# Performance work log

Measured on AMD Instinct MI355X. Metric: run time of the kernel, lower is better.

Reference implementation:

```python
import jax, jax.numpy as jnp
import numpy as np

B, F, SF = 2, 5, 15          # batch, query frames, num_shots*sframe
C, KD, VD = 1024, 128, 512   # encoder_dim, keydim, valdim
H = W = 32                   # l3 feature map (output stride 8 on 256x256)


def _conv(x, w, b, pad):
    y = jax.lax.conv_general_dilated(
        x, w, window_strides=(1, 1), padding=[(pad, pad), (pad, pad)],
        dimension_numbers=("NCHW", "OIHW", "NCHW"))
    return y + b[None, :, None, None]


def setup_inputs() -> dict:
    key = jax.random.key(0)
    ks = jax.random.split(key, 8)
    s = 0.02
    return {
        "query_feat": jax.random.normal(ks[0], (B * F, C, H, W), jnp.float32),
        "support_fg_feat": jax.random.normal(ks[1], (B * SF, C, H, W), jnp.float32),
        "w_sk": jax.random.normal(ks[2], (KD, C, 3, 3), jnp.float32) * s,
        "b_sk": jnp.zeros((KD,), jnp.float32),
        "w_sv": jax.random.normal(ks[3], (VD, C, 3, 3), jnp.float32) * s,
        "b_sv": jnp.zeros((VD,), jnp.float32),
        "w_qq": jax.random.normal(ks[4], (KD, C, 3, 3), jnp.float32) * s,
        "b_qq": jnp.zeros((KD,), jnp.float32),
        "w_qk": jax.random.normal(ks[5], (KD, C, 3, 3), jnp.float32) * s,
        "b_qk": jnp.zeros((KD,), jnp.float32),
        "w_cq": jax.random.normal(ks[6], (VD, C, 1, 1), jnp.float32) * s,
        "b_cq": jnp.zeros((VD,), jnp.float32),
    }


def reference(query_feat, support_fg_feat, w_sk, b_sk, w_sv, b_sv,
              w_qq, b_qq, w_qk, b_qk, w_cq, b_cq):
    hw = H * W
    # QKV projections (3x3 convs)
    sk = _conv(support_fg_feat, w_sk, b_sk, 1)   # [B*SF, KD, H, W]
    sv = _conv(support_fg_feat, w_sv, b_sv, 1)   # [B*SF, VD, H, W]
    qq = _conv(query_feat, w_qq, b_qq, 1)        # [B*F, KD, H, W]
    qk = _conv(query_feat, w_qk, b_qk, 1)        # [B*F, KD, H, W]

    # support K: [B, SF*hw, KD];  support V: [B, VD, SF*hw]
    support_k = sk.reshape(B, SF, KD, H, W).transpose(0, 2, 1, 3, 4)
    support_k = support_k.reshape(B, KD, SF * hw).transpose(0, 2, 1)
    support_v = sv.reshape(B, SF, VD, H, W).transpose(0, 2, 1, 3, 4)
    support_v = support_v.reshape(B, VD, SF * hw)

    qq5 = qq.reshape(B, F, KD, H, W)
    qk5 = qk.reshape(B, F, KD, H, W)
    mid = F // 2
    scale = 1.0 / jnp.sqrt(jnp.float32(KD))

    # stage 1: middle-frame query attends into support memory
    middle_q = qq5[:, mid].reshape(B, KD, hw)                 # [B, KD, hw]
    P1 = jnp.einsum("bkc,bcq->bkq", support_k, middle_q) * scale  # [B, SF*hw, hw]
    P1 = jax.nn.softmax(P1, axis=1)
    new_V = jnp.einsum("bvk,bkq->bvq", support_v, P1)          # [B, VD, hw]

    # stage 2: all-frame queries attend into middle-frame keys
    middle_K = qk5[:, mid].reshape(B, KD, hw).transpose(0, 2, 1)   # [B, hw, KD]
    qq_flat = qq5.transpose(0, 2, 1, 3, 4).reshape(B, KD, F * hw)  # [B, KD, F*hw]
    P2 = jnp.einsum("bkc,bcq->bkq", middle_K, qq_flat) * scale     # [B, hw, F*hw]
    P2 = jax.nn.softmax(P2, axis=1)
    Out = jnp.einsum("bvk,bkq->bvq", new_V, P2)                    # [B, VD, F*hw]

    after = Out.reshape(B, VD, F, H, W).transpose(0, 2, 1, 3, 4)
    after = after.reshape(B * F, VD, H, W)
    qf = _conv(query_feat, w_cq, b_cq, 0)                          # [B*F, VD, H, W]
    return jnp.concatenate([after, qf], axis=1)                    # [B*F, 2*VD, H, W]
```

## Files before the change

kernel.cpp:

```cpp
#include <hip/hip_runtime.h>
#include <cstdint>

typedef unsigned short u16;
typedef __attribute__((ext_vector_type(8))) u16 u16x8;
typedef __attribute__((ext_vector_type(4))) u16 u16x4;
typedef __attribute__((ext_vector_type(8))) _Float16 f16x8;
typedef __attribute__((ext_vector_type(4))) float f32x4;

__device__ __forceinline__ u16 f2h(float f) {
  _Float16 h = (_Float16)f;
  return __builtin_bit_cast(u16, h);
}
__device__ __forceinline__ float h2f(u16 b) {
  _Float16 h = __builtin_bit_cast(_Float16, b);
  return (float)h;
}
__device__ __forceinline__ void gll16(const void* g, void* l) {
  auto gp = reinterpret_cast<const __attribute__((address_space(1))) unsigned int*>(
      reinterpret_cast<uintptr_t>(g));
  auto lp = reinterpret_cast<__attribute__((address_space(3))) unsigned int*>(
      reinterpret_cast<uintptr_t>(l));
  __builtin_amdgcn_global_load_lds(gp, lp, 16, 0, 0);
}

__global__ __launch_bounds__(256) void pad_both(const float* __restrict__ qsrc,
                                                const float* __restrict__ ssrc,
                                                u16* __restrict__ PQ,
                                                u16* __restrict__ PS) {
  const int gi = blockIdx.x >> 5;
  const int y  = blockIdx.x & 31;
  const float* in;
  u16* outp;
  int img;
  if (gi < 10) { in = qsrc; outp = PQ; img = gi; }
  else         { in = ssrc; outp = PS; img = gi - 10; }
  __shared__ float tile[32][33];
  const int tid = threadIdx.x;
  u16* base = outp + (long)img * 34 * 34 * 1024;
  const u16x8 z8 = {0, 0, 0, 0, 0, 0, 0, 0};
  {
    u16* r = base + (long)(y + 1) * 34 * 1024;
    if (tid < 128) *(u16x8*)&r[tid * 8] = z8;
    else *(u16x8*)&r[33 * 1024 + (tid - 128) * 8] = z8;
  }
  if (y == 0) {
    for (int i = tid * 8; i < 34816; i += 2048) *(u16x8*)&base[i] = z8;
  }
  if (y == 31) {
    u16* r = base + 33L * 34 * 1024;
    for (int i = tid * 8; i < 34816; i += 2048) *(u16x8*)&r[i] = z8;
  }
  const int xi = tid & 31, ci = tid >> 5;
  const int xo = tid >> 3, q = tid & 7;
  const float* ip = in + (long)img * 1048576 + y * 32;
  u16* op = base + ((long)(y + 1) * 34 + 1) * 1024;
  for (int c0 = 0; c0 < 1024; c0 += 32) {
#pragma unroll
    for (int k2 = 0; k2 < 4; k2++)
      tile[k2 * 8 + ci][xi] = ip[(long)(c0 + k2 * 8 + ci) * 1024 + xi];
    __syncthreads();
    u16x4 o4;
#pragma unroll
    for (int r = 0; r < 4; r++) o4[r] = f2h(tile[q * 4 + r][xo]);
    *(u16x4*)&op[(long)xo * 1024 + c0 + q * 4] = o4;
    __syncthreads();
  }
}

__device__ __forceinline__ void wre3_body(const float* __restrict__ wp,
                                          u16* __restrict__ op, float* buf) {
  for (int i = threadIdx.x; i < 9216; i += 256) buf[i] = wp[i];
  __syncthreads();
  for (int k = threadIdx.x; k < 9216; k += 256) {
    const int cblk = k / 576;
    const int r = k - cblk * 576;
    const int t = r >> 6, ci = r & 63;
    op[k] = f2h(buf[(cblk * 64 + ci) * 9 + t]);
  }
}
__global__ __launch_bounds__(256) void wprep(
    const float* __restrict__ w_sk, const float* __restrict__ w_sv,
    const float* __restrict__ w_qq, const float* __restrict__ w_qk,
    const float* __restrict__ w_cq, u16* __restrict__ WTSK,
    u16* __restrict__ WTSV, u16* __restrict__ WTQQK, u16* __restrict__ WCQ) {
  __shared__ float buf[9216];
  const int b = blockIdx.x;
  if (b < 128) {
    wre3_body(w_sk + (long)b * 9216, WTSK + (long)b * 9216, buf);
  } else if (b < 640) {
    const int oc = b - 128;
    wre3_body(w_sv + (long)oc * 9216, WTSV + (long)oc * 9216, buf);
  } else if (b < 768) {
    const int oc = b - 640;
    wre3_body(w_qq + (long)oc * 9216, WTQQK + (long)oc * 9216, buf);
  } else if (b < 896) {
    const int oc = b - 768;
    wre3_body(w_qk + (long)oc * 9216, WTQQK + (long)(oc + 128) * 9216, buf);
  } else {
    const int i = (b - 896) * 1024 + threadIdx.x * 4;
#pragma unroll
    for (int r = 0; r < 4; r++) WCQ[i + r] = f2h(w_cq[i + r]);
  }
}

__global__ __launch_bounds__(64) void reduceD(const float* __restrict__ ps,
                                              float* __restrict__ D, int NT) {
  const int row = blockIdx.x, tid = threadIdx.x;
  const float* p = ps + (long)row * NT;
  float s = (tid < NT) ? p[tid] : 0.f;
  if (tid + 64 < NT) s += p[tid + 64];
#pragma unroll
  for (int o = 32; o > 0; o >>= 1) s += __shfl_xor(s, o, 64);
  if (tid == 0) D[row] = s;
}

__global__ __launch_bounds__(256) void reduce8h(const u16* __restrict__ part,
                                                const float* __restrict__ D,
                                                u16* __restrict__ o) {
  long j = ((long)blockIdx.x * 256 + threadIdx.x) * 4;
  int b = (int)(j >> 19);
  long i = j & 524287;
  int q = (int)(i & 1023);
  const u16* p = part + (long)b * 4194304 + i;
  float s0 = 0.f, s1 = 0.f, s2 = 0.f, s3 = 0.f;
#pragma unroll
  for (int c = 0; c < 8; c++) {
    u16x4 v = *(const u16x4*)&p[(long)c * 524288];
    s0 += h2f(v[0]); s1 += h2f(v[1]); s2 += h2f(v[2]); s3 += h2f(v[3]);
  }
  f32x4 dv = *(const f32x4*)&D[b * 1024 + q];
  u16x4 o4 = {f2h(s0 / dv[0]), f2h(s1 / dv[1]), f2h(s2 / dv[2]),
              f2h(s3 / dv[3])};
  *(u16x4*)&o[j] = o4;
}
__global__ __launch_bounds__(256) void reduce_sk(const u16* __restrict__ part,
                                                 const float* __restrict__ bias,
                                                 u16* __restrict__ o) {
  long i = ((long)blockIdx.x * 256 + threadIdx.x) * 4;
  u16x4 a = *(const u16x4*)&part[i];
  u16x4 b = *(const u16x4*)&part[i + 3932160];
  f32x4 bb = *(const f32x4*)&bias[(int)(i & 127)];
  u16x4 o4;
#pragma unroll
  for (int r = 0; r < 4; r++) o4[r] = f2h(h2f(a[r]) + h2f(b[r]) + bb[r]);
  *(u16x4*)&o[i] = o4;
}
__global__ __launch_bounds__(256) void reduce_qqk(
    const u16* __restrict__ part, const float* __restrict__ b_qq,
    const float* __restrict__ b_qk, u16* __restrict__ QQR,
    u16* __restrict__ QKR) {
  long i = ((long)blockIdx.x * 256 + threadIdx.x) * 4;
  const int n = (int)(i >> 8), m = (int)(i & 255);
  u16x4 a = *(const u16x4*)&part[i];
  u16x4 b = *(const u16x4*)&part[i + 2621440];
  const int lo = (m < 128);
  const int mm = m & 127;
  const float* bs = lo ? b_qq : b_qk;
  f32x4 bb = *(const f32x4*)&bs[mm];
  u16* dst = (lo ? QQR : QKR) + (long)n * 128 + mm;
  u16x4 o4;
#pragma unroll
  for (int r = 0; r < 4; r++) o4[r] = f2h(h2f(a[r]) + h2f(b[r]) + bb[r]);
  *(u16x4*)dst = o4;
}

__global__ __launch_bounds__(512, 1)
void gemm256(const u16* __restrict__ A, const u16* __restrict__ B,
             const float* __restrict__ bias, u16* __restrict__ out) {
  __shared__ u16 lds[81920];
  const int tid = threadIdx.x, lane = tid & 63, wave = tid >> 6;
  const int nwg = gridDim.x * gridDim.y;
  int wg = blockIdx.x + gridDim.x * blockIdx.y;
  wg = (wg & 7) * (nwg >> 3) + (wg >> 3);
  const int ntile = wg % gridDim.x;
  const int mtile = wg / gridDim.x;

  const int slog = (lane & 7) ^ ((lane >> 3) & 7);
  const u16* aS[4];
  const u16* bS[4];
  int aD[4], bD[4];
#pragma unroll
  for (int j = 0; j < 4; j++) {
    const int r = wave * 32 + j * 8 + (lane >> 3);
    aS[j] = A + (long)(mtile * 256 + r) * 9216 + slog * 8;
    aD[j] = (wave * 32 + j * 8) * 64;
    const int n = ntile * 256 + r;
    const int img = n >> 10, p = n & 1023;
    const int y = p >> 5, x = p & 31;
    bS[j] = B + ((long)((img * 34 + y) * 34 + x)) * 1024 + slog * 8;
    bD[j] = (wave * 32 + j * 8) * 64;
  }

  const int g = lane >> 4, l15 = lane & 15;
  const int wm = wave >> 2, wn = wave & 3;
  int aRow[8], bRow[4], sx[2];
#pragma unroll
  for (int mi = 0; mi < 8; mi++) aRow[mi] = (wm * 128 + mi * 16 + l15) * 64;
#pragma unroll
  for (int ni = 0; ni < 4; ni++) bRow[ni] = (wn * 64 + ni * 16 + l15) * 64;
#pragma unroll
  for (int ks = 0; ks < 2; ks++) sx[ks] = ((ks * 4 + g) ^ (l15 & 7)) * 8;

  auto conv_badd = [](int kt) {
    const int cblk = kt / 9;
    const int t = kt - cblk * 9;
    const int dy = t / 3, dx = t - dy * 3;
    return (dy * 34 + dx) * 1024 + cblk * 64;
  };

  f32x4 acc[8][4];
  const f32x4 zero = {0.f, 0.f, 0.f, 0.f};
#pragma unroll
  for (int i = 0; i < 8; i++)
#pragma unroll
    for (int j = 0; j < 4; j++) acc[i][j] = zero;

  const int nkt = 144;
  {
#pragma unroll
    for (int j = 0; j < 4; j++) gll16(aS[j], &lds[aD[j]]);
    const int b0o = conv_badd(0), b1o = conv_badd(1);
#pragma unroll
    for (int j = 0; j < 4; j++) gll16(bS[j] + b0o, &lds[32768 + bD[j]]);
#pragma unroll
    for (int j = 0; j < 4; j++) gll16(bS[j] + b1o, &lds[49152 + bD[j]]);
    asm volatile("s_waitcnt vmcnt(4)" ::: "memory");
    __builtin_amdgcn_s_barrier();
  }

  f16x8 a0[4], a1[4], a3[4], b0[4], b2[4];
  f16x8 zf;
#pragma unroll
  for (int j = 0; j < 8; j++) zf[j] = (_Float16)0.0f;
#pragma unroll
  for (int i = 0; i < 4; i++) { a3[i] = zf; b2[i] = zf; }

  int bc = 0;
  for (int kt = 0; kt < nkt; ++kt) {
    const int abuf = (kt & 1) << 14;
    const int anbuf = abuf ^ 16384;
    const int bbuf = 32768 + bc * 16384;
    int bsn = bc + 2; if (bsn >= 3) bsn -= 3;
    const int bnbuf = 32768 + bsn * 16384;
    const bool stA = (kt + 1 < nkt);
    const bool stB = (kt + 2 < nkt);
    const int kA = (kt + 1) << 6;
    const int bAdd2 = stB ? conv_badd(kt + 2) : 0;

#pragma unroll
    for (int i = 0; i < 4; i++) a0[i] = *(const f16x8*)&lds[abuf + aRow[i] + sx[0]];
#pragma unroll
    for (int i = 0; i < 4; i++) b0[i] = *(const f16x8*)&lds[bbuf + bRow[i] + sx[0]];
#pragma unroll
    for (int i = 0; i < 4; i++) a1[i] = *(const f16x8*)&lds[abuf + aRow[i + 4] + sx[0]];
#pragma unroll
    for (int mi = 0; mi < 4; mi++)
#pragma unroll
      for (int ni = 0; ni < 4; ni++)
        acc[mi + 4][ni] = __builtin_amdgcn_mfma_f32_16x16x32_f16(
            a3[mi], b2[ni], acc[mi + 4][ni], 0, 0, 0);
    if (stA) {
#pragma unroll
      for (int j = 0; j < 4; j++) gll16(aS[j] + kA, &lds[anbuf + aD[j]]);
    }
#pragma unroll
    for (int mi = 0; mi < 4; mi++)
#pragma unroll
      for (int ni = 0; ni < 4; ni++)
        acc[mi][ni] = __builtin_amdgcn_mfma_f32_16x16x32_f16(
            a0[mi], b0[ni], acc[mi][ni], 0, 0, 0);
#pragma unroll
    for (int i = 0; i < 4; i++) a0[i] = *(const f16x8*)&lds[abuf + aRow[i] + sx[1]];
#pragma unroll
    for (int i = 0; i < 4; i++) b2[i] = *(const f16x8*)&lds[bbuf + bRow[i] + sx[1]];
    if (stB) {
#pragma unroll
      for (int j = 0; j < 4; j++) gll16(bS[j] + bAdd2, &lds[bnbuf + bD[j]]);
    }
#pragma unroll
    for (int mi = 0; mi < 4; mi++)
#pragma unroll
      for (int ni = 0; ni < 4; ni++)
        acc[mi + 4][ni] = __builtin_amdgcn_mfma_f32_16x16x32_f16(
            a1[mi], b0[ni], acc[mi + 4][ni], 0, 0, 0);
#pragma unroll
    for (int i = 0; i < 4; i++) a3[i] = *(const f16x8*)&lds[abuf + aRow[i + 4] + sx[1]];
#pragma unroll
    for (int mi = 0; mi < 4; mi++)
#pragma unroll
      for (int ni = 0; ni < 4; ni++)
        acc[mi][ni] = __builtin_amdgcn_mfma_f32_16x16x32_f16(
            a0[mi], b2[ni], acc[mi][ni], 0, 0, 0);
    if (stB) {
      asm volatile("s_waitcnt vmcnt(4)" ::: "memory");
    } else if (stA) {
      asm volatile("s_waitcnt vmcnt(0)" ::: "memory");
    }
    __builtin_amdgcn_s_barrier();
    bc = bc + 1; if (bc >= 3) bc -= 3;
  }
#pragma unroll
  for (int mi = 0; mi < 4; mi++)
#pragma unroll
    for (int ni = 0; ni < 4; ni++)
      acc[mi + 4][ni] = __builtin_amdgcn_mfma_f32_16x16x32_f16(
          a3[mi], b2[ni], acc[mi + 4][ni], 0, 0, 0);

#pragma unroll
  for (int mi = 0; mi < 8; mi++) {
#pragma unroll
    for (int ni = 0; ni < 4; ni++) {
      f32x4 v = acc[mi][ni];
      const int m0 = mtile * 256 + wm * 128 + mi * 16 + g * 4;
      const int n = ntile * 256 + wn * 64 + ni * 16 + l15;
      const int b = (n >= 15360) ? 1 : 0;
      const int rem = n - b * 15360;
#pragma unroll
      for (int r = 0; r < 4; r++) {
        const int m = m0 + r;
        out[(long)b * 7864320 + (long)m * 15360 + rem] = f2h(v[r] + bias[m]);
      }
    }
  }
}

template <int BMODE, int EPI, int SPLITK>
__global__ __launch_bounds__(256, 2)
void gemm_nt(const u16* __restrict__ A, long Azoff, int Astride,
             const u16* __restrict__ B, long Bzoff, int Bstride,
             int K, float scale,
             const float* __restrict__ bias, const float* __restrict__ bias2,
             void* __restrict__ out0, void* __restrict__ out1,
             long out_zoff, int ldo, float cexp = 0.f) {
  __shared__ u16 lds[4 * 8192];
  const int tid = threadIdx.x;
  const int lane = tid & 63;
  const int wave = tid >> 6;
  const int mtile = blockIdx.y, ntile = blockIdx.x, z = blockIdx.z;

  const int zb = (SPLITK > 1) ? z / SPLITK : z;
  const int zc = (SPLITK > 1) ? z % SPLITK : 0;
  const u16* Ab = A + (long)zb * Azoff + (long)zc * K;
  const u16* Bb = B + (long)zb * Bzoff + ((BMODE == 0) ? (long)zc * K : 0);

  const int r8 = lane >> 3;
  const int sphys = lane & 7;
  const u16* aSrc[4];
  const u16* bSrc[4];
  u16* aDst[4];
  u16* bDst[4];
#pragma unroll
  for (int i = 0; i < 4; i++) {
    const int row = wave * 32 + i * 8 + r8;
    const int slog = sphys ^ (row & 7);
    aSrc[i] = Ab + (long)(mtile * 128 + row) * Astride + slog * 8;
    if (BMODE == 0) {
      bSrc[i] = Bb + (long)(ntile * 128 + row) * Bstride + slog * 8;
    } else {
      const int n = ntile * 128 + row;
      const int img = n >> 10;
      const int p = n & 1023;
      const int y = p >> 5, x = p & 31;
      bSrc[i] = Bb + ((long)(img * 34 + y) * 34 + x) * 1024 + slog * 8;
    }
    aDst[i] = &lds[0] + (wave * 32 + i * 8) * 64;
    bDst[i] = &lds[0] + 8192 + (wave * 32 + i * 8) * 64;
  }

  const int g = lane >> 4, l15 = lane & 15;
  const int wm = wave >> 1, wn = wave & 1;
  int offA[2][4], offB[2][4];
#pragma unroll
  for (int ks = 0; ks < 2; ks++) {
    const int sl = ks * 4 + g;
#pragma unroll
    for (int i = 0; i < 4; i++) {
      const int ra = wm * 64 + i * 16 + l15;
      offA[ks][i] = ra * 64 + ((sl ^ (ra & 7)) * 8);
      const int rb = wn * 64 + i * 16 + l15;
      offB[ks][i] = 8192 + rb * 64 + ((sl ^ (rb & 7)) * 8);
    }
  }

  auto stage = [&](int buf, int kb) {
    int bAdd;
    if (BMODE == 0) {
      bAdd = kb;
    } else if (BMODE == 1) {
      const int ktg = (zc * K + kb) >> 6;
      const int cblk = ktg / 9;
      const int t = ktg - cblk * 9;
      const int dy = t / 3, dx = t - dy * 3;
      bAdd = (dy * 34 + dx) * 1024 + cblk * 64;
    } else {
      bAdd = 35 * 1024 + kb;
    }
    const int bufo = buf * 16384;
#pragma unroll
    for (int i = 0; i < 4; i++) gll16(aSrc[i] + kb, aDst[i] + bufo);
#pragma unroll
    for (int i = 0; i < 4; i++) gll16(bSrc[i] + bAdd, bDst[i] + bufo);
  };

  f32x4 acc[4][4];
  const f32x4 zero = {0.f, 0.f, 0.f, 0.f};
#pragma unroll
  for (int i = 0; i < 4; i++)
#pragma unroll
    for (int j = 0; j < 4; j++) acc[i][j] = zero;

  const int nkt = K >> 6;
  stage(0, 0);
  __syncthreads();
  for (int kt = 0; kt < nkt; ++kt) {
    const int buf = kt & 1;
    if (kt + 1 < nkt) stage(buf ^ 1, (kt + 1) << 6);
#pragma unroll
    for (int ks = 0; ks < 2; ks++) {
      f16x8 af[4], bfg[4];
#pragma unroll
      for (int i = 0; i < 4; i++)
        af[i] = *(const f16x8*)&lds[buf * 16384 + offA[ks][i]];
#pragma unroll
      for (int i = 0; i < 4; i++)
        bfg[i] = *(const f16x8*)&lds[buf * 16384 + offB[ks][i]];
#pragma unroll
      for (int mi = 0; mi < 4; mi++)
#pragma unroll
        for (int ni = 0; ni < 4; ni++)
          acc[mi][ni] = __builtin_amdgcn_mfma_f32_16x16x32_f16(
              af[mi], bfg[ni], acc[mi][ni], 0, 0, 0);
    }
    __syncthreads();
  }

  float rp[4][4];
  if (EPI == 7) {
#pragma unroll
    for (int a = 0; a < 4; a++)
#pragma unroll
      for (int b = 0; b < 4; b++) rp[a][b] = 0.f;
  }

#pragma unroll
  for (int mi = 0; mi < 4; mi++) {
#pragma unroll
    for (int ni = 0; ni < 4; ni++) {
      f32x4 v = acc[mi][ni];
      const int m0 = mtile * 128 + wm * 64 + mi * 16 + g * 4;
      const int n = ntile * 128 + wn * 64 + ni * 16 + l15;
      if (EPI == 0) {
        u16* ob = (u16*)out0;
        const float* bs = bias;
        int mm = m0;
        if (out1 != nullptr && m0 >= 128) { ob = (u16*)out1; bs = bias2; mm = m0 - 128; }
        u16x4 pk;
#pragma unroll
        for (int r = 0; r < 4; r++) {
          float val = v[r] * scale + (bs ? bs[mm + r] : 0.f);
          pk[r] = f2h(val);
        }
        *(u16x4*)&ob[(long)n * ldo + mm] = pk;
      } else if (EPI == 1) {
        u16* ob = (u16*)out0 + (long)z * out_zoff;
#pragma unroll
        for (int r = 0; r < 4; r++) {
          const int m = m0 + r;
          float val = v[r] * scale + (bias ? bias[m] : 0.f);
          ob[(long)m * ldo + n] = f2h(val);
        }
      } else if (EPI == 2) {
        float* of = (float*)out0;
        const int img = n >> 10, p = n & 1023;
#pragma unroll
        for (int r = 0; r < 4; r++) {
          const int m = m0 + r;
          of[(long)img * 1048576 + (long)(512 + m) * 1024 + p] =
              v[r] + (bias ? bias[m] : 0.f);
        }
      } else if (EPI == 3) {
        float* of = (float*)out0;
        const int f = n >> 10, p = n & 1023;
        const float dinv = 1.0f / bias2[(long)z * 5120 + n];
#pragma unroll
        for (int r = 0; r < 4; r++) {
          const int m = m0 + r;
          of[(long)z * 5242880 + (long)f * 1048576 + (long)m * 1024 + p] =
              v[r] * dinv;
        }
      } else if (EPI == 4) {
        float* of = (float*)out0 + (long)z * out_zoff;
#pragma unroll
        for (int r = 0; r < 4; r++) of[(long)(m0 + r) * ldo + n] = v[r];
      } else if (EPI == 5) {
        float* of = (float*)out0 + (long)zc * out_zoff;
        *(f32x4*)&of[(long)n * ldo + m0] = v;
      } else if (EPI == 6) {
        u16* ob = (u16*)out0 + (long)z * out_zoff;
#pragma unroll
        for (int r = 0; r < 4; r++) ob[(long)(m0 + r) * ldo + n] = f2h(v[r]);
      } else if (EPI == 7) {
        u16* ob = (u16*)out0 + (long)z * out_zoff;
#pragma unroll
        for (int r = 0; r < 4; r++) {
          const int m = m0 + r;
          float e = __expf(v[r] * scale - cexp);
          ob[(long)m * ldo + n] = f2h(e);
          rp[mi][r] += e;
        }
      } else {
        u16* ob = (u16*)out0 + (long)zc * out_zoff;
        u16x4 pk;
#pragma unroll
        for (int r = 0; r < 4; r++) pk[r] = f2h(v[r]);
        *(u16x4*)&ob[(long)n * ldo + m0] = pk;
      }
    }
  }

  if (EPI == 7) {
    float* ps = (float*)lds;
#pragma unroll
    for (int mi = 0; mi < 4; mi++) {
#pragma unroll
      for (int r = 0; r < 4; r++) {
        float s = rp[mi][r];
        s += __shfl_xor(s, 1, 64);
        s += __shfl_xor(s, 2, 64);
        s += __shfl_xor(s, 4, 64);
        s += __shfl_xor(s, 8, 64);
        if (l15 == 0) ps[wn * 128 + wm * 64 + mi * 16 + g * 4 + r] = s;
      }
    }
    __syncthreads();
    if (tid < 128) {
      float s = ps[tid] + ps[128 + tid];
      const int MR = gridDim.y << 7;
      float* PS = (float*)out1;
      PS[((long)z * MR + mtile * 128 + tid) * gridDim.x + ntile] = s;
    }
  }
}

extern "C" void kernel_launch(void* const* d_in, const int* in_sizes, int n_in,
                              void* d_out, int out_size, void* d_ws, size_t ws_size,
                              hipStream_t stream) {
  (void)in_sizes; (void)n_in; (void)out_size;
  const float* query   = (const float*)d_in[0];
  const float* support = (const float*)d_in[1];
  const float* w_sk = (const float*)d_in[2];  const float* b_sk = (const float*)d_in[3];
  const float* w_sv = (const float*)d_in[4];  const float* b_sv = (const float*)d_in[5];
  const float* w_qq = (const float*)d_in[6];  const float* b_qq = (const float*)d_in[7];
  const float* w_qk = (const float*)d_in[8];  const float* b_qk = (const float*)d_in[9];
  const float* w_cq = (const float*)d_in[10]; const float* b_cq = (const float*)d_in[11];
  float* out = (float*)d_out;
  char* ws = (char*)d_ws;

  if (ws_size < 158924800u) return;

  u16* PQ    = (u16*)(ws + 0);
  u16* PS    = (u16*)(ws + 23674880);
  u16* WTSK  = (u16*)(ws + 94699520);
  u16* WTSV  = (u16*)(ws + 97058816);
  u16* WTQQK = (u16*)(ws + 106496000);
  u16* WCQ   = (u16*)(ws + 111214592);
  u16* SKR   = (u16*)(ws + 112263168);
  u16* SVA   = (u16*)(ws + 120127488);
  u16* QQR   = (u16*)(ws + 151584768);
  u16* QKR   = (u16*)(ws + 154206208);
  u16* NEWV  = (u16*)(ws + 156827648);
  u16* P1T   = PS;
  u16* P2T   = PQ;
  u16* PART2 = (u16*)(ws + 94699520);
  u16* PARTKH = SVA;
  u16* PARTQH = SVA;
  float* PSUM1 = (float*)(ws + 97058816);
  float* PSUM2 = (float*)(ws + 94699520);
  float* D1 = (float*)(ws + 112263168);
  float* D2 = D1 + 2048;

  const float SCALE = 0.08838834764831843f;

  pad_both<<<dim3(1280), 256, 0, stream>>>(query, support, PQ, PS);
  wprep<<<dim3(1408), 256, 0, stream>>>(w_sk, w_sv, w_qq, w_qk, w_cq,
                                        WTSK, WTSV, WTQQK, WCQ);

  gemm_nt<1, 8, 2><<<dim3(240, 1, 2), 256, 0, stream>>>(
      WTSK, 0, 9216, PS, 0, 0, 4608, 1.0f, nullptr, nullptr, PARTKH, nullptr,
      3932160L, 128);
  reduce_sk<<<dim3(3840), 256, 0, stream>>>(PARTKH, b_sk, SKR);

  gemm_nt<1, 8, 2><<<dim3(80, 2, 2), 256, 0, stream>>>(
      WTQQK, 0, 9216, PQ, 0, 0, 4608, 1.0f, nullptr, nullptr, PARTQH, nullptr,
      2621440L, 256);
  reduce_qqk<<<dim3(2560), 256, 0, stream>>>(PARTQH, b_qq, b_qk, QQR, QKR);

  gemm256<<<dim3(120, 2), 512, 0, stream>>>(WTSV, PS, b_sv, SVA);

  gemm_nt<2, 2, 1><<<dim3(80, 4, 1), 256, 0, stream>>>(
      WCQ, 0, 1024, PQ, 0, 0, 1024, 1.0f, b_cq, nullptr, out, nullptr, 0, 0);

  gemm_nt<0, 7, 1><<<dim3(120, 8, 2), 256, 0, stream>>>(
      QQR + 262144, 655360L, 128, SKR, 1966080L, 128, 128, SCALE, nullptr,
      nullptr, P1T, PSUM1, 15728640L, 15360, 12.0f);
  reduceD<<<dim3(2048), 64, 0, stream>>>(PSUM1, D1, 120);
  gemm_nt<0, 6, 8><<<dim3(8, 4, 16), 256, 0, stream>>>(
      SVA, 7864320L, 15360, P1T, 15728640L, 15360, 1920, 1.0f, nullptr,
      nullptr, PART2, nullptr, 524288L, 1024);
  reduce8h<<<dim3(1024), 256, 0, stream>>>(PART2, D1, NEWV);

  gemm_nt<0, 7, 1><<<dim3(8, 40, 2), 256, 0, stream>>>(
      QQR, 655360L, 128, QKR + 262144, 655360L, 128, 128, SCALE, nullptr,
      nullptr, P2T, PSUM2, 5242880L, 1024, 10.0f);
  reduceD<<<dim3(10240), 64, 0, stream>>>(PSUM2, D2, 8);
  gemm_nt<0, 3, 1><<<dim3(40, 4, 2), 256, 0, stream>>>(
      NEWV, 524288L, 1024, P2T, 5242880L, 1024, 1024, 1.0f, nullptr, D2,
      out, nullptr, 0, 0);
}
```

Before: 595.5 us.

## Merge independent kernel launches into combined dual-role kernels

```diff
diff --git a/kernel.cpp b/kernel.cpp
--- a/kernel.cpp
+++ b/kernel.cpp
@@ -21,50 +21,6 @@
   auto lp = reinterpret_cast<__attribute__((address_space(3))) unsigned int*>(
       reinterpret_cast<uintptr_t>(l));
   __builtin_amdgcn_global_load_lds(gp, lp, 16, 0, 0);
-}
-
-__global__ __launch_bounds__(256) void pad_both(const float* __restrict__ qsrc,
-                                                const float* __restrict__ ssrc,
-                                                u16* __restrict__ PQ,
-                                                u16* __restrict__ PS) {
-  const int gi = blockIdx.x >> 5;
-  const int y  = blockIdx.x & 31;
-  const float* in;
-  u16* outp;
-  int img;
-  if (gi < 10) { in = qsrc; outp = PQ; img = gi; }
-  else         { in = ssrc; outp = PS; img = gi - 10; }
-  __shared__ float tile[32][33];
-  const int tid = threadIdx.x;
-  u16* base = outp + (long)img * 34 * 34 * 1024;
-  const u16x8 z8 = {0, 0, 0, 0, 0, 0, 0, 0};
-  {
-    u16* r = base + (long)(y + 1) * 34 * 1024;
-    if (tid < 128) *(u16x8*)&r[tid * 8] = z8;
-    else *(u16x8*)&r[33 * 1024 + (tid - 128) * 8] = z8;
-  }
-  if (y == 0) {
-    for (int i = tid * 8; i < 34816; i += 2048) *(u16x8*)&base[i] = z8;
-  }
-  if (y == 31) {
-    u16* r = base + 33L * 34 * 1024;
-    for (int i = tid * 8; i < 34816; i += 2048) *(u16x8*)&r[i] = z8;
-  }
-  const int xi = tid & 31, ci = tid >> 5;
-  const int xo = tid >> 3, q = tid & 7;
-  const float* ip = in + (long)img * 1048576 + y * 32;
-  u16* op = base + ((long)(y + 1) * 34 + 1) * 1024;
-  for (int c0 = 0; c0 < 1024; c0 += 32) {
-#pragma unroll
-    for (int k2 = 0; k2 < 4; k2++)
-      tile[k2 * 8 + ci][xi] = ip[(long)(c0 + k2 * 8 + ci) * 1024 + xi];
-    __syncthreads();
-    u16x4 o4;
-#pragma unroll
-    for (int r = 0; r < 4; r++) o4[r] = f2h(tile[q * 4 + r][xo]);
-    *(u16x4*)&op[(long)xo * 1024 + c0 + q * 4] = o4;
-    __syncthreads();
-  }
 }
 
 __device__ __forceinline__ void wre3_body(const float* __restrict__ wp,
@@ -78,40 +34,90 @@
     op[k] = f2h(buf[(cblk * 64 + ci) * 9 + t]);
   }
 }
-__global__ __launch_bounds__(256) void wprep(
+__global__ __launch_bounds__(256) void prep_all(
+    const float* __restrict__ qsrc, const float* __restrict__ ssrc,
+    u16* __restrict__ PQ, u16* __restrict__ PS,
     const float* __restrict__ w_sk, const float* __restrict__ w_sv,
     const float* __restrict__ w_qq, const float* __restrict__ w_qk,
     const float* __restrict__ w_cq, u16* __restrict__ WTSK,
     u16* __restrict__ WTSV, u16* __restrict__ WTQQK, u16* __restrict__ WCQ) {
   __shared__ float buf[9216];
-  const int b = blockIdx.x;
-  if (b < 128) {
-    wre3_body(w_sk + (long)b * 9216, WTSK + (long)b * 9216, buf);
-  } else if (b < 640) {
-    const int oc = b - 128;
-    wre3_body(w_sv + (long)oc * 9216, WTSV + (long)oc * 9216, buf);
-  } else if (b < 768) {
-    const int oc = b - 640;
-    wre3_body(w_qq + (long)oc * 9216, WTQQK + (long)oc * 9216, buf);
-  } else if (b < 896) {
-    const int oc = b - 768;
-    wre3_body(w_qk + (long)oc * 9216, WTQQK + (long)(oc + 128) * 9216, buf);
+  const int bb = blockIdx.x;
+  if (bb < 1280) {
+    const int gi = bb >> 5;
+    const int y  = bb & 31;
+    const float* in;
+    u16* outp;
+    int img;
+    if (gi < 10) { in = qsrc; outp = PQ; img = gi; }
+    else         { in = ssrc; outp = PS; img = gi - 10; }
+    float (*tile)[33] = (float(*)[33])buf;
+    const int tid = threadIdx.x;
+    u16* base = outp + (long)img * 34 * 34 * 1024;
+    const u16x8 z8 = {0, 0, 0, 0, 0, 0, 0, 0};
+    {
+      u16* r = base + (long)(y + 1) * 34 * 1024;
+      if (tid < 128) *(u16x8*)&r[tid * 8] = z8;
+      else *(u16x8*)&r[33 * 1024 + (tid - 128) * 8] = z8;
+    }
+    if (y == 0) {
+      for (int i = tid * 8; i < 34816; i += 2048) *(u16x8*)&base[i] = z8;
+    }
+    if (y == 31) {
+      u16* r = base + 33L * 34 * 1024;
+      for (int i = tid * 8; i < 34816; i += 2048) *(u16x8*)&r[i] = z8;
+    }
+    const int xi = tid & 31, ci = tid >> 5;
+    const int xo = tid >> 3, q = tid & 7;
+    const float* ip = in + (long)img * 1048576 + y * 32;
+    u16* op = base + ((long)(y + 1) * 34 + 1) * 1024;
+    for (int c0 = 0; c0 < 1024; c0 += 32) {
+#pragma unroll
+      for (int k2 = 0; k2 < 4; k2++)
+        tile[k2 * 8 + ci][xi] = ip[(long)(c0 + k2 * 8 + ci) * 1024 + xi];
+      __syncthreads();
+      u16x4 o4;
+#pragma unroll
+      for (int r = 0; r < 4; r++) o4[r] = f2h(tile[q * 4 + r][xo]);
+      *(u16x4*)&op[(long)xo * 1024 + c0 + q * 4] = o4;
+      __syncthreads();
+    }
   } else {
-    const int i = (b - 896) * 1024 + threadIdx.x * 4;
-#pragma unroll
-    for (int r = 0; r < 4; r++) WCQ[i + r] = f2h(w_cq[i + r]);
-  }
-}
-
-__global__ __launch_bounds__(64) void reduceD(const float* __restrict__ ps,
-                                              float* __restrict__ D, int NT) {
+    const int b = bb - 1280;
+    if (b < 128) {
+      wre3_body(w_sk + (long)b * 9216, WTSK + (long)b * 9216, buf);
+    } else if (b < 640) {
+      const int oc = b - 128;
+      wre3_body(w_sv + (long)oc * 9216, WTSV + (long)oc * 9216, buf);
+    } else if (b < 768) {
+      const int oc = b - 640;
+      wre3_body(w_qq + (long)oc * 9216, WTQQK + (long)oc * 9216, buf);
+    } else if (b < 896) {
+      const int oc = b - 768;
+      wre3_body(w_qk + (long)oc * 9216, WTQQK + (long)(oc + 128) * 9216, buf);
+    } else {
+      const int i = (b - 896) * 1024 + threadIdx.x * 4;
+#pragma unroll
+      for (int r = 0; r < 4; r++) WCQ[i + r] = f2h(w_cq[i + r]);
+    }
+  }
+}
+
+__global__ __launch_bounds__(64) void reduceDx(const float* __restrict__ ps1,
+                                               float* __restrict__ D1,
+                                               const float* __restrict__ ps2,
+                                               float* __restrict__ D2) {
   const int row = blockIdx.x, tid = threadIdx.x;
-  const float* p = ps + (long)row * NT;
+  const float* p;
+  float* D;
+  int NT;
+  if (row < 2048) { p = ps1 + (long)row * 120; D = D1 + row; NT = 120; }
+  else { const int r2 = row - 2048; p = ps2 + (long)r2 * 8; D = D2 + r2; NT = 8; }
   float s = (tid < NT) ? p[tid] : 0.f;
   if (tid + 64 < NT) s += p[tid + 64];
 #pragma unroll
   for (int o = 32; o > 0; o >>= 1) s += __shfl_xor(s, o, 64);
-  if (tid == 0) D[row] = s;
+  if (tid == 0) *D = s;
 }
 
 __global__ __launch_bounds__(256) void reduce8h(const u16* __restrict__ part,
@@ -133,35 +139,37 @@
               f2h(s3 / dv[3])};
   *(u16x4*)&o[j] = o4;
 }
-__global__ __launch_bounds__(256) void reduce_sk(const u16* __restrict__ part,
-                                                 const float* __restrict__ bias,
-                                                 u16* __restrict__ o) {
-  long i = ((long)blockIdx.x * 256 + threadIdx.x) * 4;
-  u16x4 a = *(const u16x4*)&part[i];
-  u16x4 b = *(const u16x4*)&part[i + 3932160];
-  f32x4 bb = *(const f32x4*)&bias[(int)(i & 127)];
-  u16x4 o4;
-#pragma unroll
-  for (int r = 0; r < 4; r++) o4[r] = f2h(h2f(a[r]) + h2f(b[r]) + bb[r]);
-  *(u16x4*)&o[i] = o4;
-}
-__global__ __launch_bounds__(256) void reduce_qqk(
-    const u16* __restrict__ part, const float* __restrict__ b_qq,
-    const float* __restrict__ b_qk, u16* __restrict__ QQR,
-    u16* __restrict__ QKR) {
-  long i = ((long)blockIdx.x * 256 + threadIdx.x) * 4;
-  const int n = (int)(i >> 8), m = (int)(i & 255);
-  u16x4 a = *(const u16x4*)&part[i];
-  u16x4 b = *(const u16x4*)&part[i + 2621440];
-  const int lo = (m < 128);
-  const int mm = m & 127;
-  const float* bs = lo ? b_qq : b_qk;
-  f32x4 bb = *(const f32x4*)&bs[mm];
-  u16* dst = (lo ? QQR : QKR) + (long)n * 128 + mm;
-  u16x4 o4;
-#pragma unroll
-  for (int r = 0; r < 4; r++) o4[r] = f2h(h2f(a[r]) + h2f(b[r]) + bb[r]);
-  *(u16x4*)dst = o4;
+__global__ __launch_bounds__(256) void reduce_kq(
+    const u16* __restrict__ partK, const float* __restrict__ b_sk,
+    u16* __restrict__ SKR, const u16* __restrict__ partQ,
+    const float* __restrict__ b_qq, const float* __restrict__ b_qk,
+    u16* __restrict__ QQR, u16* __restrict__ QKR) {
+  int blk = blockIdx.x;
+  if (blk < 3840) {
+    long i = ((long)blk * 256 + threadIdx.x) * 4;
+    u16x4 a = *(const u16x4*)&partK[i];
+    u16x4 b = *(const u16x4*)&partK[i + 3932160];
+    f32x4 bb = *(const f32x4*)&b_sk[(int)(i & 127)];
+    u16x4 o4;
+#pragma unroll
+    for (int r = 0; r < 4; r++) o4[r] = f2h(h2f(a[r]) + h2f(b[r]) + bb[r]);
+    *(u16x4*)&SKR[i] = o4;
+  } else {
+    blk -= 3840;
+    long i = ((long)blk * 256 + threadIdx.x) * 4;
+    const int n = (int)(i >> 8), m = (int)(i & 255);
+    u16x4 a = *(const u16x4*)&partQ[i];
+    u16x4 b = *(const u16x4*)&partQ[i + 2621440];
+    const int lo = (m < 128);
+    const int mm = m & 127;
+    const float* bs = lo ? b_qq : b_qk;
+    f32x4 bb = *(const f32x4*)&bs[mm];
+    u16* dst = (lo ? QQR : QKR) + (long)n * 128 + mm;
+    u16x4 o4;
+#pragma unroll
+    for (int r = 0; r < 4; r++) o4[r] = f2h(h2f(a[r]) + h2f(b[r]) + bb[r]);
+    *(u16x4*)dst = o4;
+  }
 }
 
 __global__ __launch_bounds__(512, 1)
@@ -325,18 +333,16 @@
 }
 
 template <int BMODE, int EPI, int SPLITK>
-__global__ __launch_bounds__(256, 2)
-void gemm_nt(const u16* __restrict__ A, long Azoff, int Astride,
-             const u16* __restrict__ B, long Bzoff, int Bstride,
-             int K, float scale,
-             const float* __restrict__ bias, const float* __restrict__ bias2,
-             void* __restrict__ out0, void* __restrict__ out1,
-             long out_zoff, int ldo, float cexp = 0.f) {
-  __shared__ u16 lds[4 * 8192];
+__device__ __forceinline__ void gemm_body(
+    int mtile, int ntile, int z, int NTd, int MRd,
+    const u16* __restrict__ A, long Azoff, int Astride,
+    const u16* __restrict__ B, long Bzoff, int Bstride,
+    int K, float scale, const float* __restrict__ bias,
+    const float* __restrict__ bias2, void* __restrict__ out0,
+    void* __restrict__ out1, long out_zoff, int ldo, float cexp, u16* lds) {
   const int tid = threadIdx.x;
   const int lane = tid & 63;
   const int wave = tid >> 6;
-  const int mtile = blockIdx.y, ntile = blockIdx.x, z = blockIdx.z;
 
   const int zb = (SPLITK > 1) ? z / SPLITK : z;
   const int zc = (SPLITK > 1) ? z % SPLITK : 0;
@@ -363,8 +369,8 @@
       const int y = p >> 5, x = p & 31;
       bSrc[i] = Bb + ((long)(img * 34 + y) * 34 + x) * 1024 + slog * 8;
     }
-    aDst[i] = &lds[0] + (wave * 32 + i * 8) * 64;
-    bDst[i] = &lds[0] + 8192 + (wave * 32 + i * 8) * 64;
+    aDst[i] = lds + (wave * 32 + i * 8) * 64;
+    bDst[i] = lds + 8192 + (wave * 32 + i * 8) * 64;
   }
 
   const int g = lane >> 4, l15 = lane & 15;
@@ -449,27 +455,7 @@
       f32x4 v = acc[mi][ni];
       const int m0 = mtile * 128 + wm * 64 + mi * 16 + g * 4;
       const int n = ntile * 128 + wn * 64 + ni * 16 + l15;
-      if (EPI == 0) {
-        u16* ob = (u16*)out0;
-        const float* bs = bias;
-        int mm = m0;
-        if (out1 != nullptr && m0 >= 128) { ob = (u16*)out1; bs = bias2; mm = m0 - 128; }
-        u16x4 pk;
-#pragma unroll
-        for (int r = 0; r < 4; r++) {
-          float val = v[r] * scale + (bs ? bs[mm + r] : 0.f);
-          pk[r] = f2h(val);
-        }
-        *(u16x4*)&ob[(long)n * ldo + mm] = pk;
-      } else if (EPI == 1) {
-        u16* ob = (u16*)out0 + (long)z * out_zoff;
-#pragma unroll
-        for (int r = 0; r < 4; r++) {
-          const int m = m0 + r;
-          float val = v[r] * scale + (bias ? bias[m] : 0.f);
-          ob[(long)m * ldo + n] = f2h(val);
-        }
-      } else if (EPI == 2) {
+      if (EPI == 2) {
         float* of = (float*)out0;
         const int img = n >> 10, p = n & 1023;
 #pragma unroll
@@ -488,13 +474,6 @@
           of[(long)z * 5242880 + (long)f * 1048576 + (long)m * 1024 + p] =
               v[r] * dinv;
         }
-      } else if (EPI == 4) {
-        float* of = (float*)out0 + (long)z * out_zoff;
-#pragma unroll
-        for (int r = 0; r < 4; r++) of[(long)(m0 + r) * ldo + n] = v[r];
-      } else if (EPI == 5) {
-        float* of = (float*)out0 + (long)zc * out_zoff;
-        *(f32x4*)&of[(long)n * ldo + m0] = v;
       } else if (EPI == 6) {
         u16* ob = (u16*)out0 + (long)z * out_zoff;
 #pragma unroll
@@ -535,10 +514,62 @@
     __syncthreads();
     if (tid < 128) {
       float s = ps[tid] + ps[128 + tid];
-      const int MR = gridDim.y << 7;
-      float* PS = (float*)out1;
-      PS[((long)z * MR + mtile * 128 + tid) * gridDim.x + ntile] = s;
-    }
+      float* PSp = (float*)out1;
+      PSp[((long)z * MRd + mtile * 128 + tid) * NTd + ntile] = s;
+    }
+  }
+}
+
+template <int BMODE, int EPI, int SPLITK>
+__global__ __launch_bounds__(256, 2)
+void gemm_nt(const u16* __restrict__ A, long Azoff, int Astride,
+             const u16* __restrict__ B, long Bzoff, int Bstride,
+             int K, float scale,
+             const float* __restrict__ bias, const float* __restrict__ bias2,
+             void* __restrict__ out0, void* __restrict__ out1,
+             long out_zoff, int ldo, float cexp = 0.f) {
+  __shared__ u16 lds[32768];
+  gemm_body<BMODE, EPI, SPLITK>(blockIdx.y, blockIdx.x, blockIdx.z,
+                                gridDim.x, gridDim.y << 7, A, Azoff, Astride,
+                                B, Bzoff, Bstride, K, scale, bias, bias2,
+                                out0, out1, out_zoff, ldo, cexp, lds);
+}
+
+__global__ __launch_bounds__(256, 2)
+void conv_dual(const u16* __restrict__ WTSK, const u16* __restrict__ WTQQK,
+               const u16* __restrict__ PS, const u16* __restrict__ PQ,
+               u16* __restrict__ PARTKH, u16* __restrict__ PARTQH) {
+  __shared__ u16 lds[32768];
+  int b = blockIdx.x;
+  if (b < 480) {
+    gemm_body<1, 8, 2>(0, b % 240, b / 240, 0, 0, WTSK, 0, 9216, PS, 0, 0,
+                       4608, 1.0f, nullptr, nullptr, PARTKH, nullptr,
+                       3932160L, 128, 0.f, lds);
+  } else {
+    b -= 480;
+    gemm_body<1, 8, 2>((b / 80) % 2, b % 80, b / 160, 0, 0, WTQQK, 0, 9216,
+                       PQ, 0, 0, 4608, 1.0f, nullptr, nullptr, PARTQH,
+                       nullptr, 2621440L, 256, 0.f, lds);
+  }
+}
+
+__global__ __launch_bounds__(256, 2)
+void pgemm_dual(const u16* __restrict__ QQR, const u16* __restrict__ SKR,
+                const u16* __restrict__ QKR, u16* __restrict__ P1T,
+                u16* __restrict__ P2T, float* __restrict__ PSUM1,
+                float* __restrict__ PSUM2, float scale) {
+  __shared__ u16 lds[32768];
+  int b = blockIdx.x;
+  if (b < 1920) {
+    gemm_body<0, 7, 1>((b / 120) % 8, b % 120, b / 960, 120, 1024,
+                       QQR + 262144, 655360L, 128, SKR, 1966080L, 128, 128,
+                       scale, nullptr, nullptr, P1T, PSUM1, 15728640L, 15360,
+                       12.0f, lds);
+  } else {
+    b -= 1920;
+    gemm_body<0, 7, 1>((b / 8) % 40, b % 8, b / 320, 8, 5120, QQR, 655360L,
+                       128, QKR + 262144, 655360L, 128, 128, scale, nullptr,
+                       nullptr, P2T, PSUM2, 5242880L, 1024, 10.0f, lds);
   }
 }
 
@@ -573,7 +604,7 @@
   u16* P2T   = PQ;
   u16* PART2 = (u16*)(ws + 94699520);
   u16* PARTKH = SVA;
-  u16* PARTQH = SVA;
+  u16* PARTQH = SVA + 7864320;
   float* PSUM1 = (float*)(ws + 97058816);
   float* PSUM2 = (float*)(ws + 94699520);
   float* D1 = (float*)(ws + 112263168);
@@ -581,38 +612,28 @@
 
   const float SCALE = 0.08838834764831843f;
 
-  pad_both<<<dim3(1280), 256, 0, stream>>>(query, support, PQ, PS);
-  wprep<<<dim3(1408), 256, 0, stream>>>(w_sk, w_sv, w_qq, w_qk, w_cq,
-                                        WTSK, WTSV, WTQQK, WCQ);
-
-  gemm_nt<1, 8, 2><<<dim3(240, 1, 2), 256, 0, stream>>>(
-      WTSK, 0, 9216, PS, 0, 0, 4608, 1.0f, nullptr, nullptr, PARTKH, nullptr,
-      3932160L, 128);
-  reduce_sk<<<dim3(3840), 256, 0, stream>>>(PARTKH, b_sk, SKR);
-
-  gemm_nt<1, 8, 2><<<dim3(80, 2, 2), 256, 0, stream>>>(
-      WTQQK, 0, 9216, PQ, 0, 0, 4608, 1.0f, nullptr, nullptr, PARTQH, nullptr,
-      2621440L, 256);
-  reduce_qqk<<<dim3(2560), 256, 0, stream>>>(PARTQH, b_qq, b_qk, QQR, QKR);
+  prep_all<<<dim3(2688), 256, 0, stream>>>(query, support, PQ, PS, w_sk, w_sv,
+                                           w_qq, w_qk, w_cq, WTSK, WTSV,
+                                           WTQQK, WCQ);
+
+  conv_dual<<<dim3(800), 256, 0, stream>>>(WTSK, WTQQK, PS, PQ, PARTKH, PARTQH);
+  reduce_kq<<<dim3(6400), 256, 0, stream>>>(PARTKH, b_sk, SKR, PARTQH, b_qq,
+                                            b_qk, QQR, QKR);
 
   gemm256<<<dim3(120, 2), 512, 0, stream>>>(WTSV, PS, b_sv, SVA);
 
   gemm_nt<2, 2, 1><<<dim3(80, 4, 1), 256, 0, stream>>>(
       WCQ, 0, 1024, PQ, 0, 0, 1024, 1.0f, b_cq, nullptr, out, nullptr, 0, 0);
 
-  gemm_nt<0, 7, 1><<<dim3(120, 8, 2), 256, 0, stream>>>(
-      QQR + 262144, 655360L, 128, SKR, 1966080L, 128, 128, SCALE, nullptr,
-      nullptr, P1T, PSUM1, 15728640L, 15360, 12.0f);
-  reduceD<<<dim3(2048), 64, 0, stream>>>(PSUM1, D1, 120);
+  pgemm_dual<<<dim3(2560), 256, 0, stream>>>(QQR, SKR, QKR, P1T, P2T, PSUM1,
+                                             PSUM2, SCALE);
+  reduceDx<<<dim3(12288), 64, 0, stream>>>(PSUM1, D1, PSUM2, D2);
+
   gemm_nt<0, 6, 8><<<dim3(8, 4, 16), 256, 0, stream>>>(
       SVA, 7864320L, 15360, P1T, 15728640L, 15360, 1920, 1.0f, nullptr,
       nullptr, PART2, nullptr, 524288L, 1024);
   reduce8h<<<dim3(1024), 256, 0, stream>>>(PART2, D1, NEWV);
 
-  gemm_nt<0, 7, 1><<<dim3(8, 40, 2), 256, 0, stream>>>(
-      QQR, 655360L, 128, QKR + 262144, 655360L, 128, 128, SCALE, nullptr,
-      nullptr, P2T, PSUM2, 5242880L, 1024, 10.0f);
-  reduceD<<<dim3(10240), 64, 0, stream>>>(PSUM2, D2, 8);
   gemm_nt<0, 3, 1><<<dim3(40, 4, 2), 256, 0, stream>>>(
       NEWV, 524288L, 1024, P2T, 5242880L, 1024, 1024, 1.0f, nullptr, D2,
       out, nullptr, 0, 0);
```

Result: faster. 581.4 us (-2.4%).
